# Optimization experiments

Measured on AMD Instinct MI355X. Metric: run time of the kernel, lower is better.

Reference implementation:

```python
import jax, jax.numpy as jnp
import numpy as np

N, CIN, DIM, H, W = 16, 256, 32, 128, 128
NUMANGLE, NUMRHO = 192, 192
BN_EPS = 1e-5


def _conv(x, w, b, pad):
    y = jax.lax.conv_general_dilated(
        x, w, window_strides=(1, 1), padding=[(pad, pad), (pad, pad)],
        dimension_numbers=("NCHW", "OIHW", "NCHW"))
    return y + b[None, :, None, None]


def _bn_relu(x, gamma, beta):
    # training-mode batchnorm (batch statistics), as nn.BatchNorm2d in train()
    m = jnp.mean(x, axis=(0, 2, 3), keepdims=True)
    v = jnp.var(x, axis=(0, 2, 3), keepdims=True)
    y = (x - m) * jax.lax.rsqrt(v + BN_EPS)
    return jax.nn.relu(y * gamma[None, :, None, None] + beta[None, :, None, None])


def _rho_index():
    # LUT exactly as in the deep-hough-transform CUDA kernel
    irho = float(int(np.sqrt(H * H + W * W) + 1)) / (NUMRHO - 1)
    theta = np.arange(NUMANGLE) * (np.pi / NUMANGLE)
    tab_sin = np.sin(theta) / irho
    tab_cos = np.cos(theta) / irho
    xx = np.arange(W) - W // 2          # center-relative integer coords
    yy = np.arange(H) - H // 2
    # r[a, y, x] = round(x'*cos/irho + y'*sin/irho) + numrho/2
    r = np.round(xx[None, None, :] * tab_cos[:, None, None]
                 + yy[None, :, None] * tab_sin[:, None, None]).astype(np.int32)
    r = np.clip(r + NUMRHO // 2, 0, NUMRHO - 1)
    return jnp.asarray(r.reshape(NUMANGLE, H * W))  # [A, P]


_RHO_IDX = _rho_index()


def _dht(feat):
    # feat: [N, C, H, W] -> accumulator [N, C, numangle, numrho]
    n, c = feat.shape[0], feat.shape[1]
    feat_f = feat.reshape(n * c, H * W).T  # [P, N*C]

    def per_angle(idx):  # idx: [P] -> [numrho, N*C]
        return jax.ops.segment_sum(feat_f, idx, num_segments=NUMRHO)

    acc = jax.vmap(per_angle)(_RHO_IDX)  # [A, R, N*C]
    return acc.transpose(2, 0, 1).reshape(n, c, NUMANGLE, NUMRHO)


def setup_inputs() -> dict:
    key = jax.random.key(0)
    ks = jax.random.split(key, 8)
    s1 = 1.0 / np.sqrt(CIN)
    s3 = 1.0 / np.sqrt(DIM * 9)
    return {
        "x": jax.random.normal(ks[0], (N, CIN, H, W), jnp.float32),
        "w1": jax.random.normal(ks[1], (DIM, CIN, 1, 1), jnp.float32) * s1,
        "b1": jnp.zeros((DIM,), jnp.float32),
        "g1": jnp.ones((DIM,), jnp.float32),
        "be1": jnp.zeros((DIM,), jnp.float32),
        "w2": jax.random.normal(ks[2], (DIM, DIM, 3, 3), jnp.float32) * s3,
        "b2": jnp.zeros((DIM,), jnp.float32),
        "g2": jnp.ones((DIM,), jnp.float32),
        "be2": jnp.zeros((DIM,), jnp.float32),
        "w3": jax.random.normal(ks[3], (DIM, DIM, 3, 3), jnp.float32) * s3,
        "b3": jnp.zeros((DIM,), jnp.float32),
        "g3": jnp.ones((DIM,), jnp.float32),
        "be3": jnp.zeros((DIM,), jnp.float32),
    }


def reference(x, w1, b1, g1, be1, w2, b2, g2, be2, w3, b3, g3, be3):
    h = _bn_relu(_conv(x, w1, b1, 0), g1, be1)      # 1x1 conv + BN + ReLU
    a = _dht(h)                                      # deep Hough transform
    h = _bn_relu(_conv(a, w2, b2, 1), g2, be2)      # 3x3 conv + BN + ReLU
    h = _bn_relu(_conv(h, w3, b3, 1), g3, be3)      # 3x3 conv + BN + ReLU
    return h
```

## Files before the change

kernel.cpp:

```cpp
#include <hip/hip_runtime.h>
#include <hip/hip_fp16.h>
#include <math.h>

#define N_    16
#define CIN_  256
#define DIM_  32
#define H_    128
#define W_    128
#define P_    (H_*W_)
#define A_    192
#define R_    192
#define AR_   (A_*R_)
#define CSR_CAP 18432
#define NWORD 16520
#define SENT  16512

struct alignas(8) h4 { __half2 a, b; };

__device__ __forceinline__ int swz(int p) {
    int y = p >> 7, x = p & 127;
    return y * 129 + (x ^ ((y & 7) << 2));
}

__global__ __launch_bounds__(256) void csr_build(
        unsigned short* __restrict__ pix, int* __restrict__ offg) {
    int a = blockIdx.x;
    __shared__ int cnt[192];
    __shared__ int off[193];
    __shared__ unsigned char rho_s[P_];
    double theta = (double)a * (M_PI / 192.0);
    double irho  = 182.0 / 191.0;
    double ts = sin(theta) / irho;
    double tc = cos(theta) / irho;
    for (int i = threadIdx.x; i < 192; i += 256) cnt[i] = 0;
    __syncthreads();
    for (int p = threadIdx.x; p < P_; p += 256) {
        int y = p >> 7, x = p & 127;
        double v = __dadd_rn(__dmul_rn((double)(x - 64), tc),
                             __dmul_rn((double)(y - 64), ts));
        int r = (int)rint(v) + 96;
        r = r < 0 ? 0 : (r > 191 ? 191 : r);
        rho_s[p] = (unsigned char)r;
        atomicAdd(&cnt[r], 1);
    }
    __syncthreads();
    if (threadIdx.x == 0) {
        int run = 0;
        for (int r = 0; r < 192; ++r) { off[r] = run; run += (cnt[r] + 3) & ~3; }
        off[192] = run;
    }
    __syncthreads();
    if (threadIdx.x < 193) offg[a * 193 + threadIdx.x] = off[threadIdx.x];
    for (int i = threadIdx.x; i < 192; i += 256) cnt[i] = off[i];
    __syncthreads();
    unsigned short* pa = pix + (size_t)a * CSR_CAP;
    for (int p = threadIdx.x; p < P_; p += 256) {
        int idx = atomicAdd(&cnt[rho_s[p]], 1);
        pa[idx] = (unsigned short)swz(p);
    }
    __syncthreads();
    for (int r = threadIdx.x; r < 192; r += 256)
        for (int j = cnt[r]; j < off[r + 1]; ++j) pa[j] = SENT;
}

__global__ __launch_bounds__(256) void conv1x1_kernel(
        const float* __restrict__ x, const float* __restrict__ w,
        const float* __restrict__ b, float* __restrict__ out) {
    int g = blockIdx.x * 256 + threadIdx.x;
    int n = g >> 14, p = g & (P_ - 1);
    const float* xp = x + (size_t)n * CIN_ * P_ + p;
    float acc[DIM_];
    #pragma unroll
    for (int co = 0; co < DIM_; ++co) acc[co] = b[co];
    for (int ci = 0; ci < CIN_; ++ci) {
        float v = xp[(size_t)ci * P_];
        #pragma unroll
        for (int co = 0; co < DIM_; ++co)
            acc[co] += v * w[co * CIN_ + ci];
    }
    float* op = out + (size_t)n * DIM_ * P_ + p;
    #pragma unroll
    for (int co = 0; co < DIM_; ++co) op[(size_t)co * P_] = acc[co];
}

__global__ __launch_bounds__(256) void stats_kernel(
        const float* __restrict__ in, int S,
        double* __restrict__ dsum, double* __restrict__ dsq) {
    int c = blockIdx.x & 31;
    const float* p = in + (size_t)blockIdx.x * S;
    double s = 0.0, q = 0.0;
    for (int i = threadIdx.x; i < S; i += 256) {
        double v = (double)p[i];
        s += v; q += v * v;
    }
    #pragma unroll
    for (int off = 32; off > 0; off >>= 1) {
        s += __shfl_down(s, off, 64);
        q += __shfl_down(q, off, 64);
    }
    __shared__ double ls[4], lq[4];
    int wv = threadIdx.x >> 6;
    if ((threadIdx.x & 63) == 0) { ls[wv] = s; lq[wv] = q; }
    __syncthreads();
    if (threadIdx.x == 0) {
        s = ls[0] + ls[1] + ls[2] + ls[3];
        q = lq[0] + lq[1] + lq[2] + lq[3];
        atomicAdd(&dsum[c], s);
        atomicAdd(&dsq[c], q);
    }
}

__global__ void fin_kernel(const double* __restrict__ dsum, const double* __restrict__ dsq,
                           const float* __restrict__ g, const float* __restrict__ be,
                           double cnt, float* __restrict__ scsh) {
    int c = threadIdx.x;
    if (c < 32) {
        double m = dsum[c] / cnt;
        double v = dsq[c] / cnt - m * m;
        double rstd = 1.0 / sqrt(v + 1e-5);
        double sc = (double)g[c] * rstd;
        scsh[c]      = (float)sc;
        scsh[32 + c] = (float)((double)be[c] - m * sc);
    }
}

__global__ __launch_bounds__(1024) void dht_gather(
        const float* __restrict__ feat, const unsigned short* __restrict__ pix,
        const int* __restrict__ offg, const float* __restrict__ scsh,
        float one, float* __restrict__ acc) {
    extern __shared__ h4 d[];
    int quad = blockIdx.x >> 1, ah = blockIdx.x & 1;
    int nc0 = quad * 4;
    {
        int cb = nc0 & 31;
        float s0 = scsh[cb],     h0 = scsh[32 + cb];
        float s1 = scsh[cb + 1], h1 = scsh[33 + cb];
        float s2 = scsh[cb + 2], h2 = scsh[34 + cb];
        float s3 = scsh[cb + 3], h3 = scsh[35 + cb];
        const float4* f0p = (const float4*)(feat + (size_t)(nc0 + 0) * P_);
        const float4* f1p = (const float4*)(feat + (size_t)(nc0 + 1) * P_);
        const float4* f2p = (const float4*)(feat + (size_t)(nc0 + 2) * P_);
        const float4* f3p = (const float4*)(feat + (size_t)(nc0 + 3) * P_);
        for (int q = threadIdx.x; q < P_ / 4; q += 1024) {
            float4 a0 = f0p[q], a1 = f1p[q], a2 = f2p[q], a3 = f3p[q];
            int p = q * 4;
            int base = swz(p);
            h4 w;
            w.a = __halves2half2(__float2half(fmaxf(a0.x * s0 + h0, 0.f)),
                                 __float2half(fmaxf(a1.x * s1 + h1, 0.f)));
            w.b = __halves2half2(__float2half(fmaxf(a2.x * s2 + h2, 0.f)),
                                 __float2half(fmaxf(a3.x * s3 + h3, 0.f)));
            d[base + 0] = w;
            w.a = __halves2half2(__float2half(fmaxf(a0.y * s0 + h0, 0.f)),
                                 __float2half(fmaxf(a1.y * s1 + h1, 0.f)));
            w.b = __halves2half2(__float2half(fmaxf(a2.y * s2 + h2, 0.f)),
                                 __float2half(fmaxf(a3.y * s3 + h3, 0.f)));
            d[base + 1] = w;
            w.a = __halves2half2(__float2half(fmaxf(a0.z * s0 + h0, 0.f)),
                                 __float2half(fmaxf(a1.z * s1 + h1, 0.f)));
            w.b = __halves2half2(__float2half(fmaxf(a2.z * s2 + h2, 0.f)),
                                 __float2half(fmaxf(a3.z * s3 + h3, 0.f)));
            d[base + 2] = w;
            w.a = __halves2half2(__float2half(fmaxf(a0.w * s0 + h0, 0.f)),
                                 __float2half(fmaxf(a1.w * s1 + h1, 0.f)));
            w.b = __halves2half2(__float2half(fmaxf(a2.w * s2 + h2, 0.f)),
                                 __float2half(fmaxf(a3.w * s3 + h3, 0.f)));
            d[base + 3] = w;
        }
        if (threadIdx.x < 8) {
            *(uint2*)&d[SENT + threadIdx.x] = make_uint2(0u, 0u);
        }
    }
    __syncthreads();
    int abase = ah * 96;
    for (int it = 0; it < 18; ++it) {
        int seg = it * 1024 + threadIdx.x;
        int al = seg / 192, r = seg - al * 192;
        int a = abase + al;
        int o0 = offg[a * 193 + r];
        int o1 = offg[a * 193 + r + 1];
        const unsigned short* pl = pix + (size_t)a * CSR_CAP;
        float s0 = 0.f, s1 = 0.f, s2 = 0.f, s3 = 0.f;
        int j = o0;
        for (; j + 8 <= o1; j += 8) {
            ushort4 ua = *(const ushort4*)(pl + j);
            ushort4 ub = *(const ushort4*)(pl + j + 4);
            h4 v0 = d[ua.x];
            h4 v1 = d[ua.y];
            h4 v2 = d[ua.z];
            h4 v3 = d[ua.w];
            h4 v4 = d[ub.x];
            h4 v5 = d[ub.y];
            h4 v6 = d[ub.z];
            h4 v7 = d[ub.w];
            s0 += __low2float(v0.a) * one; s1 += __high2float(v0.a) * one;
            s2 += __low2float(v0.b) * one; s3 += __high2float(v0.b) * one;
            s0 += __low2float(v1.a) * one; s1 += __high2float(v1.a) * one;
            s2 += __low2float(v1.b) * one; s3 += __high2float(v1.b) * one;
            s0 += __low2float(v2.a) * one; s1 += __high2float(v2.a) * one;
            s2 += __low2float(v2.b) * one; s3 += __high2float(v2.b) * one;
            s0 += __low2float(v3.a) * one; s1 += __high2float(v3.a) * one;
            s2 += __low2float(v3.b) * one; s3 += __high2float(v3.b) * one;
            s0 += __low2float(v4.a) * one; s1 += __high2float(v4.a) * one;
            s2 += __low2float(v4.b) * one; s3 += __high2float(v4.b) * one;
            s0 += __low2float(v5.a) * one; s1 += __high2float(v5.a) * one;
            s2 += __low2float(v5.b) * one; s3 += __high2float(v5.b) * one;
            s0 += __low2float(v6.a) * one; s1 += __high2float(v6.a) * one;
            s2 += __low2float(v6.b) * one; s3 += __high2float(v6.b) * one;
            s0 += __low2float(v7.a) * one; s1 += __high2float(v7.a) * one;
            s2 += __low2float(v7.b) * one; s3 += __high2float(v7.b) * one;
        }
        if (j < o1) {
            ushort4 ua = *(const ushort4*)(pl + j);
            h4 v0 = d[ua.x];
            h4 v1 = d[ua.y];
            h4 v2 = d[ua.z];
            h4 v3 = d[ua.w];
            s0 += __low2float(v0.a) * one; s1 += __high2float(v0.a) * one;
            s2 += __low2float(v0.b) * one; s3 += __high2float(v0.b) * one;
            s0 += __low2float(v1.a) * one; s1 += __high2float(v1.a) * one;
            s2 += __low2float(v1.b) * one; s3 += __high2float(v1.b) * one;
            s0 += __low2float(v2.a) * one; s1 += __high2float(v2.a) * one;
            s2 += __low2float(v2.b) * one; s3 += __high2float(v2.b) * one;
            s0 += __low2float(v3.a) * one; s1 += __high2float(v3.a) * one;
            s2 += __low2float(v3.b) * one; s3 += __high2float(v3.b) * one;
        }
        size_t ob = (size_t)nc0 * AR_ + (size_t)a * R_ + r;
        acc[ob]           = s0;
        acc[ob + AR_]     = s1;
        acc[ob + 2 * AR_] = s2;
        acc[ob + 3 * AR_] = s3;
    }
}

template <bool BN>
__global__ __launch_bounds__(256) void conv3x3_kernel(
        const float* __restrict__ in, const float* __restrict__ w,
        const float* __restrict__ b,
        const float* __restrict__ sc, const float* __restrict__ sh,
        float* __restrict__ out) {
    __shared__ float tile[18][20];
    int tx = threadIdx.x & 15, ty = threadIdx.x >> 4;
    int x0 = blockIdx.x * 16, y0 = blockIdx.y * 16, n = blockIdx.z;
    float acc[DIM_];
    #pragma unroll
    for (int co = 0; co < DIM_; ++co) acc[co] = b[co];

    for (int ci = 0; ci < DIM_; ++ci) {
        __syncthreads();
        const float* src = in + ((size_t)(n * DIM_ + ci)) * AR_;
        float csc = BN ? sc[ci] : 0.f, csh = BN ? sh[ci] : 0.f;
        for (int t = threadIdx.x; t < 18 * 18; t += 256) {
            int ly = t / 18, lx = t - ly * 18;
            int gy = y0 - 1 + ly, gx = x0 - 1 + lx;
            float v = 0.f;
            if (gy >= 0 && gy < 192 && gx >= 0 && gx < 192) {
                v = src[gy * 192 + gx];
                if (BN) v = fmaxf(v * csc + csh, 0.f);
            }
            tile[ly][lx] = v;
        }
        __syncthreads();
        float v[9];
        #pragma unroll
        for (int k = 0; k < 9; ++k) v[k] = tile[ty + k / 3][tx + k % 3];
        const float* wp = w + ci * 9;
        #pragma unroll
        for (int co = 0; co < DIM_; ++co) {
            #pragma unroll
            for (int k = 0; k < 9; ++k)
                acc[co] += v[k] * wp[co * 288 + k];
        }
    }
    size_t o = ((size_t)(n * DIM_) * 192 + (y0 + ty)) * 192 + x0 + tx;
    #pragma unroll
    for (int co = 0; co < DIM_; ++co) out[o + (size_t)co * AR_] = acc[co];
}

__global__ __launch_bounds__(256) void bnrelu_kernel(
        const float* __restrict__ in, const float* __restrict__ scsh,
        float* __restrict__ out) {
    int i = blockIdx.x * 256 + threadIdx.x;
    if (i >= 4718592) return;
    int c = (i / 9216) & 31;
    float sc = scsh[c], sh = scsh[32 + c];
    float4 v = ((const float4*)in)[i];
    v.x = fmaxf(v.x * sc + sh, 0.f);
    v.y = fmaxf(v.y * sc + sh, 0.f);
    v.z = fmaxf(v.z * sc + sh, 0.f);
    v.w = fmaxf(v.w * sc + sh, 0.f);
    ((float4*)out)[i] = v;
}

extern "C" void kernel_launch(void* const* d_in, const int* in_sizes, int n_in,
                              void* d_out, int out_size, void* d_ws, size_t ws_size,
                              hipStream_t stream) {
    const float* x   = (const float*)d_in[0];
    const float* w1  = (const float*)d_in[1];
    const float* b1  = (const float*)d_in[2];
    const float* g1  = (const float*)d_in[3];
    const float* be1 = (const float*)d_in[4];
    const float* w2  = (const float*)d_in[5];
    const float* b2  = (const float*)d_in[6];
    const float* g2  = (const float*)d_in[7];
    const float* be2 = (const float*)d_in[8];
    const float* w3  = (const float*)d_in[9];
    const float* b3  = (const float*)d_in[10];
    const float* g3  = (const float*)d_in[11];
    const float* be3 = (const float*)d_in[12];
    float* out = (float*)d_out;

    char* ws = (char*)d_ws;
    float* bufA = (float*)(ws);
    unsigned short* pix = (unsigned short*)(ws + 33554432);
    int*   offg  = (int*)(ws + 40632320);
    float* bufB  = (float*)(ws + 75497472);
    double* stats = (double*)(ws + 150994944);
    float*  scsh  = (float*)(ws + 150996480);

    hipMemsetAsync(stats, 0, 192 * sizeof(double), stream);
    csr_build<<<192, 256, 0, stream>>>(pix, offg);

    conv1x1_kernel<<<1024, 256, 0, stream>>>(x, w1, b1, bufA);
    stats_kernel<<<512, 256, 0, stream>>>(bufA, P_, stats + 0, stats + 32);
    fin_kernel<<<1, 64, 0, stream>>>(stats + 0, stats + 32, g1, be1,
                                     (double)(N_ * P_), scsh);

    hipFuncSetAttribute((const void*)dht_gather,
                        hipFuncAttributeMaxDynamicSharedMemorySize,
                        NWORD * sizeof(h4));
    dht_gather<<<256, 1024, NWORD * sizeof(h4), stream>>>(
        bufA, pix, offg, scsh, 1.0f, bufB);

    conv3x3_kernel<false><<<dim3(12, 12, 16), 256, 0, stream>>>(
        bufB, w2, b2, nullptr, nullptr, bufA);
    stats_kernel<<<512, 256, 0, stream>>>(bufA, AR_, stats + 64, stats + 96);
    fin_kernel<<<1, 64, 0, stream>>>(stats + 64, stats + 96, g2, be2,
                                     (double)(N_ * AR_), scsh + 64);

    conv3x3_kernel<true><<<dim3(12, 12, 16), 256, 0, stream>>>(
        bufA, w3, b3, scsh + 64, scsh + 96, bufB);
    stats_kernel<<<512, 256, 0, stream>>>(bufB, AR_, stats + 128, stats + 160);
    fin_kernel<<<1, 64, 0, stream>>>(stats + 128, stats + 160, g3, be3,
                                     (double)(N_ * AR_), scsh + 128);

    bnrelu_kernel<<<18432, 256, 0, stream>>>(bufB, scsh + 128, out);
}
```

Measured before the change: 1.351 ms.

## Pre-sum gathered Hough values in half2 and batch conv3x3 channel staging

```diff
diff --git a/kernel.cpp b/kernel.cpp
--- a/kernel.cpp
+++ b/kernel.cpp
@@ -193,22 +193,14 @@
             h4 v5 = d[ub.y];
             h4 v6 = d[ub.z];
             h4 v7 = d[ub.w];
-            s0 += __low2float(v0.a) * one; s1 += __high2float(v0.a) * one;
-            s2 += __low2float(v0.b) * one; s3 += __high2float(v0.b) * one;
-            s0 += __low2float(v1.a) * one; s1 += __high2float(v1.a) * one;
-            s2 += __low2float(v1.b) * one; s3 += __high2float(v1.b) * one;
-            s0 += __low2float(v2.a) * one; s1 += __high2float(v2.a) * one;
-            s2 += __low2float(v2.b) * one; s3 += __high2float(v2.b) * one;
-            s0 += __low2float(v3.a) * one; s1 += __high2float(v3.a) * one;
-            s2 += __low2float(v3.b) * one; s3 += __high2float(v3.b) * one;
-            s0 += __low2float(v4.a) * one; s1 += __high2float(v4.a) * one;
-            s2 += __low2float(v4.b) * one; s3 += __high2float(v4.b) * one;
-            s0 += __low2float(v5.a) * one; s1 += __high2float(v5.a) * one;
-            s2 += __low2float(v5.b) * one; s3 += __high2float(v5.b) * one;
-            s0 += __low2float(v6.a) * one; s1 += __high2float(v6.a) * one;
-            s2 += __low2float(v6.b) * one; s3 += __high2float(v6.b) * one;
-            s0 += __low2float(v7.a) * one; s1 += __high2float(v7.a) * one;
-            s2 += __low2float(v7.b) * one; s3 += __high2float(v7.b) * one;
+            __half2 ta = __hadd2(__hadd2(v0.a, v1.a), __hadd2(v2.a, v3.a));
+            __half2 tb = __hadd2(__hadd2(v0.b, v1.b), __hadd2(v2.b, v3.b));
+            s0 += __low2float(ta) * one; s1 += __high2float(ta) * one;
+            s2 += __low2float(tb) * one; s3 += __high2float(tb) * one;
+            ta = __hadd2(__hadd2(v4.a, v5.a), __hadd2(v6.a, v7.a));
+            tb = __hadd2(__hadd2(v4.b, v5.b), __hadd2(v6.b, v7.b));
+            s0 += __low2float(ta) * one; s1 += __high2float(ta) * one;
+            s2 += __low2float(tb) * one; s3 += __high2float(tb) * one;
         }
         if (j < o1) {
             ushort4 ua = *(const ushort4*)(pl + j);
@@ -216,14 +208,10 @@
             h4 v1 = d[ua.y];
             h4 v2 = d[ua.z];
             h4 v3 = d[ua.w];
-            s0 += __low2float(v0.a) * one; s1 += __high2float(v0.a) * one;
-            s2 += __low2float(v0.b) * one; s3 += __high2float(v0.b) * one;
-            s0 += __low2float(v1.a) * one; s1 += __high2float(v1.a) * one;
-            s2 += __low2float(v1.b) * one; s3 += __high2float(v1.b) * one;
-            s0 += __low2float(v2.a) * one; s1 += __high2float(v2.a) * one;
-            s2 += __low2float(v2.b) * one; s3 += __high2float(v2.b) * one;
-            s0 += __low2float(v3.a) * one; s1 += __high2float(v3.a) * one;
-            s2 += __low2float(v3.b) * one; s3 += __high2float(v3.b) * one;
+            __half2 ta = __hadd2(__hadd2(v0.a, v1.a), __hadd2(v2.a, v3.a));
+            __half2 tb = __hadd2(__hadd2(v0.b, v1.b), __hadd2(v2.b, v3.b));
+            s0 += __low2float(ta) * one; s1 += __high2float(ta) * one;
+            s2 += __low2float(tb) * one; s3 += __high2float(tb) * one;
         }
         size_t ob = (size_t)nc0 * AR_ + (size_t)a * R_ + r;
         acc[ob]           = s0;
@@ -239,37 +227,42 @@
         const float* __restrict__ b,
         const float* __restrict__ sc, const float* __restrict__ sh,
         float* __restrict__ out) {
-    __shared__ float tile[18][20];
+    __shared__ float tile[16][18][20];
     int tx = threadIdx.x & 15, ty = threadIdx.x >> 4;
     int x0 = blockIdx.x * 16, y0 = blockIdx.y * 16, n = blockIdx.z;
     float acc[DIM_];
     #pragma unroll
     for (int co = 0; co < DIM_; ++co) acc[co] = b[co];
 
-    for (int ci = 0; ci < DIM_; ++ci) {
+    for (int half = 0; half < 2; ++half) {
+        int cb = half * 16;
         __syncthreads();
-        const float* src = in + ((size_t)(n * DIM_ + ci)) * AR_;
-        float csc = BN ? sc[ci] : 0.f, csh = BN ? sh[ci] : 0.f;
-        for (int t = threadIdx.x; t < 18 * 18; t += 256) {
-            int ly = t / 18, lx = t - ly * 18;
-            int gy = y0 - 1 + ly, gx = x0 - 1 + lx;
-            float v = 0.f;
-            if (gy >= 0 && gy < 192 && gx >= 0 && gx < 192) {
-                v = src[gy * 192 + gx];
-                if (BN) v = fmaxf(v * csc + csh, 0.f);
+        for (int ci = 0; ci < 16; ++ci) {
+            const float* src = in + ((size_t)(n * DIM_ + cb + ci)) * AR_;
+            float csc = BN ? sc[cb + ci] : 0.f, csh = BN ? sh[cb + ci] : 0.f;
+            for (int t = threadIdx.x; t < 324; t += 256) {
+                int ly = t / 18, lx = t - ly * 18;
+                int gy = y0 - 1 + ly, gx = x0 - 1 + lx;
+                float v = 0.f;
+                if (gy >= 0 && gy < 192 && gx >= 0 && gx < 192) {
+                    v = src[gy * 192 + gx];
+                    if (BN) v = fmaxf(v * csc + csh, 0.f);
+                }
+                tile[ci][ly][lx] = v;
             }
-            tile[ly][lx] = v;
         }
         __syncthreads();
-        float v[9];
-        #pragma unroll
-        for (int k = 0; k < 9; ++k) v[k] = tile[ty + k / 3][tx + k % 3];
-        const float* wp = w + ci * 9;
-        #pragma unroll
-        for (int co = 0; co < DIM_; ++co) {
+        for (int ci = 0; ci < 16; ++ci) {
+            float v[9];
             #pragma unroll
-            for (int k = 0; k < 9; ++k)
-                acc[co] += v[k] * wp[co * 288 + k];
+            for (int k = 0; k < 9; ++k) v[k] = tile[ci][ty + k / 3][tx + k % 3];
+            const float* wp = w + (cb + ci) * 9;
+            #pragma unroll
+            for (int co = 0; co < DIM_; ++co) {
+                #pragma unroll
+                for (int k = 0; k < 9; ++k)
+                    acc[co] += v[k] * wp[co * 288 + k];
+            }
         }
     }
     size_t o = ((size_t)(n * DIM_) * 192 + (y0 + ty)) * 192 + x0 + tx;
```

New measurement: 1.456 ms. 1.08x slower.
